# Performance work log

Hardware: AMD Instinct MI355X
Metric: run time of the kernel (lower is better)

## Reference

```python
import jax, jax.numpy as jnp
import numpy as np

N_NODES = 50000
N_EDGES = 1_250_000
D_FEAT = 64


def setup_inputs() -> dict:
    key = jax.random.key(0)
    k_seq, k_rows, k_cols, k_vals = jax.random.split(key, 4)
    seq = jax.random.normal(k_seq, (1, N_NODES, D_FEAT), dtype=jnp.float32)
    rows = jnp.sort(jax.random.randint(k_rows, (N_EDGES,), 0, N_NODES, dtype=jnp.int32))
    cols = jax.random.randint(k_cols, (N_EDGES,), 0, N_NODES, dtype=jnp.int32)
    vals = jax.random.uniform(k_vals, (N_EDGES,), dtype=jnp.float32)
    return {"seq": seq, "vals": vals, "rows": rows, "cols": cols}


def reference(seq, vals, rows, cols):
    # torch.spmm(adj, seq.squeeze(0)) with adj in COO form (rows, cols, vals):
    # out[r] = sum_{e: rows[e]==r} vals[e] * seq[0, cols[e], :]
    x = jnp.squeeze(seq, 0)                      # [N, D]
    gathered = x[cols] * vals[:, None]           # [E, D] gather + scale
    out = jax.ops.segment_sum(gathered, rows, num_segments=N_NODES)  # [N, D]
    return out[None]                             # unsqueeze(0) -> [1, N, D]
```

## Files before the change

### kernel.cpp

```cpp
#include <hip/hip_runtime.h>


#define WPB 4

__global__ __launch_bounds__(256) void row_ptr_kernel(
    const int* __restrict__ rows, int* __restrict__ row_start,
    int n_edges, int n_nodes)
{
    const int e = blockIdx.x * blockDim.x + threadIdx.x;
    if (e >= n_edges) return;
    const int r    = rows[e];
    const int prev = (e == 0) ? -1 : rows[e - 1];
    for (int t = prev + 1; t <= r; ++t) row_start[t] = e;
    if (e == n_edges - 1)
        for (int t = r + 1; t <= n_nodes; ++t) row_start[t] = n_edges;
}

__global__ __launch_bounds__(256) void spmm_kernel(
    const float4* __restrict__ seq,
    const float* __restrict__ vals,
    const int*   __restrict__ cols,
    const int*   __restrict__ row_start,
    float*       __restrict__ out,
    int n_nodes, int n_edges)
{
    const int lane = threadIdx.x & 63;
    const int sub  = lane >> 4;
    const int fl   = lane & 15;
    const int ml   = fl & 7;
    const int wave = blockIdx.x * WPB + (threadIdx.x >> 6);

    const int r = wave * 4 + sub;
    if (wave * 4 >= n_nodes) return;
    const bool valid = (r < n_nodes);

    int e = 0, e_end = 0;
    if (valid) {
        e     = row_start[r];
        e_end = row_start[r + 1];
    }

    float4 acc = make_float4(0.f, 0.f, 0.f, 0.f);

    while (__any(e < e_end)) {
        int cidx = e + ml;
        if (cidx >= n_edges) cidx = n_edges - 1;
        const int   c = cols[cidx];
        const float v = vals[cidx];

        float4 x[8];
#pragma unroll
        for (int u = 0; u < 8; ++u) {
            const int cu = __shfl(c, (sub << 4) | u);
            if (e + u < e_end)
                x[u] = seq[(cu << 4) + fl];
        }
#pragma unroll
        for (int u = 0; u < 8; ++u) {
            const float vu = __shfl(v, (sub << 4) | u);
            if (e + u < e_end) {
                acc.x = fmaf(vu, x[u].x, acc.x);
                acc.y = fmaf(vu, x[u].y, acc.y);
                acc.z = fmaf(vu, x[u].z, acc.z);
                acc.w = fmaf(vu, x[u].w, acc.w);
            }
        }
        e += 8;
    }

    if (valid)
        ((float4*)out)[(r << 4) + fl] = acc;
}

extern "C" void kernel_launch(void* const* d_in, const int* in_sizes, int n_in,
                              void* d_out, int out_size, void* d_ws, size_t ws_size,
                              hipStream_t stream) {
    const float* seq  = (const float*)d_in[0];
    const float* vals = (const float*)d_in[1];
    const int*   rows = (const int*)d_in[2];
    const int*   cols = (const int*)d_in[3];
    float*       out  = (float*)d_out;

    const int n_edges = in_sizes[1];
    const int n_nodes = out_size / 64;

    int* row_start = (int*)d_ws;

    {
        const int threads = 256;
        const int blocks  = (n_edges + threads - 1) / threads;
        row_ptr_kernel<<<blocks, threads, 0, stream>>>(rows, row_start,
                                                       n_edges, n_nodes);
    }
    {
        const int waves  = (n_nodes + 3) / 4;
        const int blocks = (waves + WPB - 1) / WPB;
        spmm_kernel<<<blocks, 256, 0, stream>>>(
            (const float4*)seq, vals, cols, row_start, out,
            n_nodes, n_edges);
    }
}
```

Before: 117.4 us.

## Replace row-pointer prepass kernel with in-kernel binary search over sorted rows

Removes the separate row_ptr kernel that scanned all edges to build CSR offsets, and instead has each wave binary-search the sorted rows array for its five row boundaries, shuffling them to the four sub-groups. This drops one kernel launch and a full pass over the rows array plus its workspace writes and reads. In exchange every wave performs about 21 dependent global loads for the search, which adds latency at the start of each wave, though the upper levels of the search should stay cached.

```diff
diff --git a/kernel.cpp b/kernel.cpp
--- a/kernel.cpp
+++ b/kernel.cpp
@@ -3,24 +3,11 @@
 
 #define WPB 4
 
-__global__ __launch_bounds__(256) void row_ptr_kernel(
-    const int* __restrict__ rows, int* __restrict__ row_start,
-    int n_edges, int n_nodes)
-{
-    const int e = blockIdx.x * blockDim.x + threadIdx.x;
-    if (e >= n_edges) return;
-    const int r    = rows[e];
-    const int prev = (e == 0) ? -1 : rows[e - 1];
-    for (int t = prev + 1; t <= r; ++t) row_start[t] = e;
-    if (e == n_edges - 1)
-        for (int t = r + 1; t <= n_nodes; ++t) row_start[t] = n_edges;
-}
-
 __global__ __launch_bounds__(256) void spmm_kernel(
     const float4* __restrict__ seq,
     const float* __restrict__ vals,
     const int*   __restrict__ cols,
-    const int*   __restrict__ row_start,
+    const int*   __restrict__ rows,
     float*       __restrict__ out,
     int n_nodes, int n_edges)
 {
@@ -30,21 +17,31 @@
     const int ml   = fl & 7;
     const int wave = blockIdx.x * WPB + (threadIdx.x >> 6);
 
-    const int r = wave * 4 + sub;
-    if (wave * 4 >= n_nodes) return;
+    const int base = wave * 4;
+    if (base >= n_nodes) return;
+
+    int target = base + (lane < 4 ? lane : 4);
+    if (target > n_nodes) target = n_nodes;
+    int lo = 0, hi = n_edges;
+    while (lo < hi) {
+        const int mid = (lo + hi) >> 1;
+        if (rows[mid] < target) lo = mid + 1;
+        else                    hi = mid;
+    }
+
+    const int r = base + sub;
     const bool valid = (r < n_nodes);
 
-    int e = 0, e_end = 0;
-    if (valid) {
-        e     = row_start[r];
-        e_end = row_start[r + 1];
-    }
+    int e     = __shfl(lo, sub);
+    int e_end = __shfl(lo, sub + 1);
+    if (!valid) { e = 0; e_end = 0; }
 
     float4 acc = make_float4(0.f, 0.f, 0.f, 0.f);
 
     while (__any(e < e_end)) {
         int cidx = e + ml;
         if (cidx >= n_edges) cidx = n_edges - 1;
+        if (cidx < 0)        cidx = 0;
         const int   c = cols[cidx];
         const float v = vals[cidx];
 
@@ -84,19 +81,8 @@
     const int n_edges = in_sizes[1];
     const int n_nodes = out_size / 64;
 
-    int* row_start = (int*)d_ws;
-
-    {
-        const int threads = 256;
-        const int blocks  = (n_edges + threads - 1) / threads;
-        row_ptr_kernel<<<blocks, threads, 0, stream>>>(rows, row_start,
-                                                       n_edges, n_nodes);
-    }
-    {
-        const int waves  = (n_nodes + 3) / 4;
-        const int blocks = (waves + WPB - 1) / WPB;
-        spmm_kernel<<<blocks, 256, 0, stream>>>(
-            (const float4*)seq, vals, cols, row_start, out,
-            n_nodes, n_edges);
-    }
+    const int waves  = (n_nodes + 3) / 4;
+    const int blocks = (waves + WPB - 1) / WPB;
+    spmm_kernel<<<blocks, 256, 0, stream>>>(
+        (const float4*)seq, vals, cols, rows, out, n_nodes, n_edges);
 }
```

After: 122.0 us. 3.9% more time.
